# Kernel optimization log

Measured on AMD Instinct MI355X. Metric: run time of the kernel, lower is better.

## Reference

```python
import jax, jax.numpy as jnp
import numpy as np

D = 256   # feature_dim
NQ = 512  # num query keypoints
NK = 512  # num key/value keypoints


def setup_inputs() -> dict:
    key = jax.random.key(0)
    ks = jax.random.split(key, 10)
    def w(k, shape, fan_in):
        return jax.random.normal(k, shape, dtype=jnp.float32) / np.sqrt(fan_in)
    inp = {
        "x": jax.random.normal(ks[0], (1, D, NQ), dtype=jnp.float32),
        "source": jax.random.normal(ks[1], (1, D, NK), dtype=jnp.float32),
        # MLPAttention score MLP: Conv1d(2D->D,k=1), ReLU, Conv1d(D->1,k=1)
        "w1": w(ks[2], (D, 2 * D), 2 * D),
        "b1": w(ks[3], (D,), 2 * D),
        "w2": w(ks[4], (1, D), D),
        "b2": w(ks[5], (1,), D),
        # outer MLP: Conv1d(2D->2D,k=1), ReLU, Conv1d(2D->D,k=1) with zero bias init
        "wa": w(ks[6], (2 * D, 2 * D), 2 * D),
        "ba": w(ks[7], (2 * D,), 2 * D),
        "wb": w(ks[8], (D, 2 * D), 2 * D),
        "bb": jnp.zeros((D,), dtype=jnp.float32),
    }
    return inp


def reference(x, source, w1, b1, w2, b2, wa, ba, wb, bb):
    d = x.shape[1]
    q = x[0]       # [D, nq]
    k = source[0]  # [D, nk]
    # cat((q broadcast over nk, k broadcast over nq)) then Conv1d(2D->D) is
    # equivalent to splitting w1 into query/key halves and broadcasting:
    w1q, w1k = w1[:, :d], w1[:, d:]
    aq = w1q @ q + b1[:, None]                       # [D, nq]
    ak = w1k @ k                                     # [D, nk]
    h = jax.nn.relu(aq[:, :, None] + ak[:, None, :])  # [D, nq, nk]
    scores = (jnp.einsum('d,dnm->nm', w2[0], h) + b2[0])[None]  # [1, nq, nk]
    prob = jax.nn.softmax(scores, axis=-1)
    message = jnp.einsum('bnm,bdm->bdn', prob, source)  # [1, D, nq]
    # outer MLP on cat([x, message], channel dim)
    cat = jnp.concatenate([x, message], axis=1)         # [1, 2D, nq]
    h2 = jax.nn.relu(jnp.einsum('oc,bcn->bon', wa, cat) + ba[None, :, None])
    y = jnp.einsum('oc,bcn->bon', wb, h2) + bb[None, :, None]  # [1, D, nq]
    return (y, scores)
```

## Files before the change

kernel.cpp:

```cpp
#include <hip/hip_runtime.h>
#include <hip/hip_bf16.h>

#define DD 256
#define NN 512

typedef __attribute__((ext_vector_type(8))) short short8;
typedef __attribute__((ext_vector_type(4))) float floatx4;

__device__ __forceinline__ unsigned short f2bf(float f) {
  unsigned u = __float_as_uint(f);
  u += 0x7FFFu + ((u >> 16) & 1u);
  return (unsigned short)(u >> 16);
}
__device__ __forceinline__ unsigned pack2(float a, float b) {
  return (unsigned)f2bf(a) | ((unsigned)f2bf(b) << 16);
}

__device__ __forceinline__ short8 ldfrag(const unsigned short* __restrict__ base,
                                         int row, int ld, int k, int lane) {
  return *(const short8*)(base + (row + (lane & 15)) * ld + k + ((lane >> 4) << 3));
}

__device__ __forceinline__ short8 ldfrag_f32(const float* __restrict__ base,
                                             int row, int ld, int k, int lane) {
  const float* p = base + (row + (lane & 15)) * ld + k + ((lane >> 4) << 3);
  const float4 v0 = *(const float4*)p;
  const float4 v1 = *(const float4*)(p + 4);
  short8 r;
  r[0] = (short)f2bf(v0.x); r[1] = (short)f2bf(v0.y);
  r[2] = (short)f2bf(v0.z); r[3] = (short)f2bf(v0.w);
  r[4] = (short)f2bf(v1.x); r[5] = (short)f2bf(v1.y);
  r[6] = (short)f2bf(v1.z); r[7] = (short)f2bf(v1.w);
  return r;
}

__device__ __forceinline__ short8 ldfragT_g(const float* __restrict__ base,
                                            int n0, int ld, int k, int lane) {
  const int n = n0 + (lane & 15);
  const int kk = k + ((lane >> 4) << 3);
  short8 r;
#pragma unroll
  for (int j = 0; j < 8; ++j) r[j] = (short)f2bf(base[(kk + j) * ld + n]);
  return r;
}

template <int NF>
__device__ __forceinline__ void acc_zero(floatx4 acc[NF]) {
#pragma unroll
  for (int i = 0; i < NF; ++i) {
    acc[i][0] = 0.f; acc[i][1] = 0.f; acc[i][2] = 0.f; acc[i][3] = 0.f;
  }
}

template <int NF>
__device__ __forceinline__ void ksplit_combine(floatx4 acc[NF], float* red,
                                               int wave, int lane) {
  const int W = 16 * NF;
  const int col = lane & 15;
  const int q = lane >> 4;
  if (wave > 0) {
    float* base = red + (wave - 1) * 16 * W;
#pragma unroll
    for (int nf = 0; nf < NF; ++nf)
#pragma unroll
      for (int r = 0; r < 4; ++r)
        base[(q * 4 + r) * W + nf * 16 + col] = acc[nf][r];
  }
  __syncthreads();
  if (wave == 0) {
#pragma unroll
    for (int nf = 0; nf < NF; ++nf)
#pragma unroll
      for (int r = 0; r < 4; ++r) {
        const int idx = (q * 4 + r) * W + nf * 16 + col;
        acc[nf][r] += red[idx] + red[16 * W + idx] + red[32 * W + idx];
      }
  }
}

template <int NF, bool COLBIAS, bool ROWBIAS, bool RELU, bool OUTBF>
__device__ __forceinline__ void gemm_epi(floatx4 acc[NF],
    const float* __restrict__ bias, void* __restrict__ C, int ldc,
    int m0, int n0, int lane) {
  const int col = lane & 15;
  const int q = lane >> 4;
#pragma unroll
  for (int nf = 0; nf < NF; ++nf) {
    const int n = n0 + nf * 16 + col;
    const float cb = COLBIAS ? bias[n] : 0.0f;
#pragma unroll
    for (int r = 0; r < 4; ++r) {
      const int m = m0 + q * 4 + r;
      float v = acc[nf][r] + cb + (ROWBIAS ? bias[m] : 0.0f);
      if (RELU) v = fmaxf(v, 0.0f);
      if (OUTBF) ((unsigned short*)C)[m * ldc + n] = f2bf(v);
      else       ((float*)C)[m * ldc + n] = v;
    }
  }
}

__global__ __launch_bounds__(256) void aqak_kernel(
    const float* __restrict__ x, const float* __restrict__ src,
    const float* __restrict__ w1, const float* __restrict__ b1,
    const float* __restrict__ bb,
    float* __restrict__ aq, float* __restrict__ ak, float* __restrict__ y,
    unsigned short* __restrict__ xT) {
  __shared__ float red[1536];

  const int tid = threadIdx.x;
  const int z = blockIdx.z;

  if (z == 2) {
    const int c = blockIdx.y * 16 + blockIdx.x;
    const float bv = bb[c];
    float2 v; v.x = bv; v.y = bv;
    *(float2*)&y[c * NN + tid * 2] = v;
    const int n0t = c * 2 + (tid >> 7);
    const int d2 = (tid & 127) * 2;
    const float f0 = x[d2 * NN + n0t];
    const float f1 = x[(d2 + 1) * NN + n0t];
    *(unsigned*)&xT[n0t * DD + d2] = pack2(f0, f1);
    return;
  }

  const int lane = tid & 63;
  const int wave = tid >> 6;
  const int m0 = blockIdx.y * 16;
  const int n0 = blockIdx.x * 32;
  const float* in = z ? src : x;

  floatx4 acc[2]; acc_zero<2>(acc);
#pragma unroll
  for (int kc = 0; kc < 2; ++kc) {
    const int kl = wave * 64 + kc * 32;
    short8 a = ldfrag_f32(w1, m0, NN, z * 256 + kl, lane);
#pragma unroll
    for (int nf = 0; nf < 2; ++nf) {
      short8 b = ldfragT_g(in, n0 + nf * 16, NN, kl, lane);
      acc[nf] = __builtin_amdgcn_mfma_f32_16x16x32_bf16(a, b, acc[nf], 0, 0, 0);
    }
  }
  ksplit_combine<2>(acc, red, wave, lane);
  if (wave == 0) {
    if (z == 0) gemm_epi<2, false, true, false, false>(acc, b1, aq, NN, m0, n0, lane);
    else        gemm_epi<2, false, false, false, false>(acc, nullptr, ak, NN, m0, n0, lane);
  }
}

__global__ __launch_bounds__(256) void scores_kernel(
    const float* __restrict__ aq, const float* __restrict__ ak,
    const float* __restrict__ w2, const float* __restrict__ b2,
    float* __restrict__ sc) {
  __shared__ __align__(16) float aqs[256][36];
  __shared__ __align__(16) float aks[256][36];
  __shared__ __align__(16) float part[4][32][32];
  __shared__ float w2s[DD];

  const int tid = threadIdx.x;
  const int lane = tid & 63;
  const int wave = tid >> 6;
  const int n0 = blockIdx.x * 32;
  const int m0 = blockIdx.y * 32;

  w2s[tid] = w2[tid];

#pragma unroll
  for (int i = 0; i < 8; ++i) {
    const int idx = i * 256 + tid;
    const int row = idx >> 3;
    const int c4 = (idx & 7) * 4;
    *(float4*)&aqs[row][c4] = *(const float4*)&aq[row * NN + n0 + c4];
    *(float4*)&aks[row][c4] = *(const float4*)&ak[row * NN + m0 + c4];
  }
  __syncthreads();

  {
    const int nq = lane & 7;
    const int mq = lane >> 3;
    float s[4][4];
#pragma unroll
    for (int i = 0; i < 4; ++i)
#pragma unroll
      for (int j = 0; j < 4; ++j) s[i][j] = 0.f;

    const int dbeg = wave * 64;
    for (int dd = dbeg; dd < dbeg + 64; ++dd) {
      const float4 a4 = *(const float4*)&aqs[dd][nq * 4];
      const float4 k4 = *(const float4*)&aks[dd][mq * 4];
      const float w = w2s[dd];
      const float a[4] = {a4.x, a4.y, a4.z, a4.w};
      const float k[4] = {k4.x, k4.y, k4.z, k4.w};
#pragma unroll
      for (int i = 0; i < 4; ++i)
#pragma unroll
        for (int j = 0; j < 4; ++j)
          s[i][j] += w * fmaxf(a[i] + k[j], 0.f);
    }
#pragma unroll
    for (int i = 0; i < 4; ++i) {
      float4 o; o.x = s[i][0]; o.y = s[i][1]; o.z = s[i][2]; o.w = s[i][3];
      *(float4*)&part[wave][nq * 4 + i][mq * 4] = o;
    }
  }
  __syncthreads();

  {
    const int n = tid >> 3;
    const int mg = (tid & 7) * 4;
    const float4 p0 = *(const float4*)&part[0][n][mg];
    const float4 p1 = *(const float4*)&part[1][n][mg];
    const float4 p2 = *(const float4*)&part[2][n][mg];
    const float4 p3 = *(const float4*)&part[3][n][mg];
    const float bv = b2[0];
    float4 o;
    o.x = p0.x + p1.x + p2.x + p3.x + bv;
    o.y = p0.y + p1.y + p2.y + p3.y + bv;
    o.z = p0.z + p1.z + p2.z + p3.z + bv;
    o.w = p0.w + p1.w + p2.w + p3.w + bv;
    *(float4*)&sc[(n0 + n) * NN + m0 + mg] = o;
  }
}

__global__ __launch_bounds__(256) void msgT_kernel(
    const float* __restrict__ sc, const float* __restrict__ srcf,
    unsigned short* __restrict__ msgTb) {
  __shared__ unsigned short Ap[16][520];
  __shared__ float red[1536];
  __shared__ float smax[16][16];
  __shared__ float ssum[16][16];
  __shared__ float rst[16][2];

  const int tid = threadIdx.x;
  const int lane = tid & 63;
  const int wave = tid >> 6;
  const int n0 = blockIdx.y * 16;
  const int d0 = blockIdx.x * 32;

  const int r = tid >> 4;
  const int c = tid & 15;
  float4 v[8];
  const float* rp = sc + (n0 + r) * NN + c * 4;
#pragma unroll
  for (int i = 0; i < 8; ++i) v[i] = *(const float4*)(rp + i * 64);

  float mx = -3.0e38f;
#pragma unroll
  for (int i = 0; i < 8; ++i)
    mx = fmaxf(mx, fmaxf(fmaxf(v[i].x, v[i].y), fmaxf(v[i].z, v[i].w)));
  smax[r][c] = mx;
  __syncthreads();
  if (c == 0) {
    float m2 = smax[r][0];
#pragma unroll
    for (int i = 1; i < 16; ++i) m2 = fmaxf(m2, smax[r][i]);
    rst[r][0] = m2;
  }
  __syncthreads();
  mx = rst[r][0];

  float sum = 0.f;
#pragma unroll
  for (int i = 0; i < 8; ++i) {
    v[i].x = __expf(v[i].x - mx); v[i].y = __expf(v[i].y - mx);
    v[i].z = __expf(v[i].z - mx); v[i].w = __expf(v[i].w - mx);
    sum += v[i].x + v[i].y + v[i].z + v[i].w;
  }
  ssum[r][c] = sum;
  __syncthreads();
  if (c == 0) {
    float s2 = ssum[r][0];
#pragma unroll
    for (int i = 1; i < 16; ++i) s2 += ssum[r][i];
    rst[r][1] = s2;
  }
  __syncthreads();
  const float inv = 1.0f / rst[r][1];
#pragma unroll
  for (int i = 0; i < 8; ++i) {
    *(unsigned*)&Ap[r][c * 4 + i * 64]     = pack2(v[i].x * inv, v[i].y * inv);
    *(unsigned*)&Ap[r][c * 4 + i * 64 + 2] = pack2(v[i].z * inv, v[i].w * inv);
  }
  __syncthreads();

  floatx4 acc[2]; acc_zero<2>(acc);
  const int k0w = wave * 128;
  const int arow = lane & 15;
  const int koff = (lane >> 4) << 3;
#pragma unroll
  for (int k = 0; k < 128; k += 32) {
    short8 a = *(const short8*)&Ap[arow][k0w + k + koff];
#pragma unroll
    for (int nf = 0; nf < 2; ++nf) {
      short8 b = ldfrag_f32(srcf, d0 + nf * 16, NN, k0w + k, lane);
      acc[nf] = __builtin_amdgcn_mfma_f32_16x16x32_bf16(a, b, acc[nf], 0, 0, 0);
    }
  }
  ksplit_combine<2>(acc, red, wave, lane);
  if (wave == 0)
    gemm_epi<2, false, false, false, true>(acc, nullptr, msgTb, DD, n0, d0, lane);
}

__global__ __launch_bounds__(256) void h2y_kernel(
    const unsigned short* __restrict__ xT, const unsigned short* __restrict__ msgTb,
    const float* __restrict__ waf, const float* __restrict__ wbf,
    const float* __restrict__ ba, float* __restrict__ y) {
  __shared__ __align__(16) unsigned short h2L[16][72];

  const int tid = threadIdx.x;
  const int lane = tid & 63;
  const int wave = tid >> 6;
  const int o0 = blockIdx.x * 64;
  const int n0g = blockIdx.y * 16;

  {
    floatx4 acc;
    acc[0] = 0.f; acc[1] = 0.f; acc[2] = 0.f; acc[3] = 0.f;
    const int ow = o0 + wave * 16;
#pragma unroll
    for (int kc = 0; kc < 16; ++kc) {
      const int c0 = kc * 32;
      short8 a = (c0 < 256) ? ldfrag(xT, n0g, DD, c0, lane)
                            : ldfrag(msgTb, n0g, DD, c0 - 256, lane);
      short8 b = ldfrag_f32(waf, ow, NN, c0, lane);
      acc = __builtin_amdgcn_mfma_f32_16x16x32_bf16(a, b, acc, 0, 0, 0);
    }
    const int col = lane & 15, q = lane >> 4;
    const float cb = ba[o0 + wave * 16 + col];
#pragma unroll
    for (int r = 0; r < 4; ++r)
      h2L[q * 4 + r][wave * 16 + col] = f2bf(fmaxf(acc[r] + cb, 0.f));
  }
  __syncthreads();

  {
    const int brow = lane & 15;
    const int koff = (lane >> 4) << 3;
    const int col = lane & 15, q = lane >> 4;
#pragma unroll
    for (int t = 0; t < 4; ++t) {
      const int o2t = wave * 64 + t * 16;
      floatx4 acc;
      acc[0] = 0.f; acc[1] = 0.f; acc[2] = 0.f; acc[3] = 0.f;
#pragma unroll
      for (int kc = 0; kc < 2; ++kc) {
        short8 a = ldfrag_f32(wbf, o2t, NN, o0 + kc * 32, lane);
        short8 b = *(const short8*)&h2L[brow][kc * 32 + koff];
        acc = __builtin_amdgcn_mfma_f32_16x16x32_bf16(a, b, acc, 0, 0, 0);
      }
#pragma unroll
      for (int r = 0; r < 4; ++r)
        atomicAdd(&y[(o2t + q * 4 + r) * NN + n0g + col], acc[r]);
    }
  }
}

extern "C" void kernel_launch(void* const* d_in, const int* in_sizes, int n_in,
                              void* d_out, int out_size, void* d_ws, size_t ws_size,
                              hipStream_t stream) {
  (void)in_sizes; (void)n_in; (void)out_size; (void)ws_size;

  const float* x   = (const float*)d_in[0];
  const float* src = (const float*)d_in[1];
  const float* w1  = (const float*)d_in[2];
  const float* b1  = (const float*)d_in[3];
  const float* w2  = (const float*)d_in[4];
  const float* b2  = (const float*)d_in[5];
  const float* wa  = (const float*)d_in[6];
  const float* ba  = (const float*)d_in[7];
  const float* wb  = (const float*)d_in[8];
  const float* bb  = (const float*)d_in[9];

  float* y_out  = (float*)d_out;
  float* sc_out = (float*)d_out + 131072;

  char* ws = (char*)d_ws;
  float*          aq    = (float*)(ws);
  float*          ak    = (float*)(ws + (512 << 10));
  unsigned short* msgTb = (unsigned short*)(ws + (1024 << 10));
  unsigned short* xT    = (unsigned short*)(ws + (1280 << 10));

  aqak_kernel<<<dim3(16, 16, 3), 256, 0, stream>>>(x, src, w1, b1, bb, aq, ak,
                                                   y_out, xT);
  scores_kernel<<<dim3(16, 16), 256, 0, stream>>>(aq, ak, w2, b2, sc_out);
  msgT_kernel<<<dim3(8, 32), 256, 0, stream>>>(sc_out, src, msgTb);
  h2y_kernel<<<dim3(8, 32), 256, 0, stream>>>(xT, msgTb, wa, wb, ba, y_out);
}
```

Measured before the change: 104.7 us.

## Fuse four kernels into one cooperative kernel with grid-wide syncs

Merges the aqak, scores, softmax/message and outer-MLP kernels into one persistent cooperative kernel of 256 blocks. Stages are separated by grid.sync(), and shared memory is reused through a union. The goal is to remove three kernel launch gaps and their launch overhead. In exchange it adds the cost of grid barriers and fixes parallelism at 256 blocks, where the first stage previously launched 768.

```diff
diff --git a/kernel.cpp b/kernel.cpp
--- a/kernel.cpp
+++ b/kernel.cpp
@@ -1,5 +1,8 @@
 #include <hip/hip_runtime.h>
 #include <hip/hip_bf16.h>
+#include <hip/hip_cooperative_groups.h>
+
+namespace cg = cooperative_groups;
 
 #define DD 256
 #define NN 512
@@ -99,257 +102,254 @@
   }
 }
 
-__global__ __launch_bounds__(256) void aqak_kernel(
+union SMem {
+  float red[1536];
+  struct {
+    float aqs[256][36];
+    float aks[256][36];
+    float part[4][32][32];
+    float w2s[DD];
+  } s2;
+  struct {
+    unsigned short Ap[16][520];
+    float red[1536];
+    float smax[16][16];
+    float ssum[16][16];
+    float rst[16][2];
+  } s3;
+  unsigned short h2L[16][72];
+};
+
+__global__ __launch_bounds__(256) void fused_kernel(
     const float* __restrict__ x, const float* __restrict__ src,
     const float* __restrict__ w1, const float* __restrict__ b1,
-    const float* __restrict__ bb,
-    float* __restrict__ aq, float* __restrict__ ak, float* __restrict__ y,
-    unsigned short* __restrict__ xT) {
-  __shared__ float red[1536];
+    const float* __restrict__ w2, const float* __restrict__ b2,
+    const float* __restrict__ wa, const float* __restrict__ ba,
+    const float* __restrict__ wb, const float* __restrict__ bb,
+    float* __restrict__ y, float* __restrict__ sc,
+    float* __restrict__ aq, float* __restrict__ ak,
+    unsigned short* __restrict__ msgTb, unsigned short* __restrict__ xT) {
+  __shared__ __align__(16) SMem sm;
+  cg::grid_group grid = cg::this_grid();
 
   const int tid = threadIdx.x;
-  const int z = blockIdx.z;
-
-  if (z == 2) {
-    const int c = blockIdx.y * 16 + blockIdx.x;
-    const float bv = bb[c];
-    float2 v; v.x = bv; v.y = bv;
-    *(float2*)&y[c * NN + tid * 2] = v;
-    const int n0t = c * 2 + (tid >> 7);
+  const int b = blockIdx.x;
+  const int lane = tid & 63;
+  const int wave = tid >> 6;
+
+  {
+    const float bv = bb[b];
+    float2 v2; v2.x = bv; v2.y = bv;
+    *(float2*)&y[b * NN + tid * 2] = v2;
+    const int n0t = b * 2 + (tid >> 7);
     const int d2 = (tid & 127) * 2;
     const float f0 = x[d2 * NN + n0t];
     const float f1 = x[(d2 + 1) * NN + n0t];
     *(unsigned*)&xT[n0t * DD + d2] = pack2(f0, f1);
-    return;
-  }
-
-  const int lane = tid & 63;
-  const int wave = tid >> 6;
-  const int m0 = blockIdx.y * 16;
-  const int n0 = blockIdx.x * 32;
-  const float* in = z ? src : x;
-
-  floatx4 acc[2]; acc_zero<2>(acc);
-#pragma unroll
-  for (int kc = 0; kc < 2; ++kc) {
-    const int kl = wave * 64 + kc * 32;
-    short8 a = ldfrag_f32(w1, m0, NN, z * 256 + kl, lane);
-#pragma unroll
-    for (int nf = 0; nf < 2; ++nf) {
-      short8 b = ldfragT_g(in, n0 + nf * 16, NN, kl, lane);
-      acc[nf] = __builtin_amdgcn_mfma_f32_16x16x32_bf16(a, b, acc[nf], 0, 0, 0);
-    }
-  }
-  ksplit_combine<2>(acc, red, wave, lane);
-  if (wave == 0) {
-    if (z == 0) gemm_epi<2, false, true, false, false>(acc, b1, aq, NN, m0, n0, lane);
-    else        gemm_epi<2, false, false, false, false>(acc, nullptr, ak, NN, m0, n0, lane);
-  }
-}
-
-__global__ __launch_bounds__(256) void scores_kernel(
-    const float* __restrict__ aq, const float* __restrict__ ak,
-    const float* __restrict__ w2, const float* __restrict__ b2,
-    float* __restrict__ sc) {
-  __shared__ __align__(16) float aqs[256][36];
-  __shared__ __align__(16) float aks[256][36];
-  __shared__ __align__(16) float part[4][32][32];
-  __shared__ float w2s[DD];
-
-  const int tid = threadIdx.x;
-  const int lane = tid & 63;
-  const int wave = tid >> 6;
-  const int n0 = blockIdx.x * 32;
-  const int m0 = blockIdx.y * 32;
-
-  w2s[tid] = w2[tid];
-
-#pragma unroll
-  for (int i = 0; i < 8; ++i) {
-    const int idx = i * 256 + tid;
-    const int row = idx >> 3;
-    const int c4 = (idx & 7) * 4;
-    *(float4*)&aqs[row][c4] = *(const float4*)&aq[row * NN + n0 + c4];
-    *(float4*)&aks[row][c4] = *(const float4*)&ak[row * NN + m0 + c4];
-  }
-  __syncthreads();
-
-  {
-    const int nq = lane & 7;
-    const int mq = lane >> 3;
-    float s[4][4];
-#pragma unroll
-    for (int i = 0; i < 4; ++i)
-#pragma unroll
-      for (int j = 0; j < 4; ++j) s[i][j] = 0.f;
-
-    const int dbeg = wave * 64;
-    for (int dd = dbeg; dd < dbeg + 64; ++dd) {
-      const float4 a4 = *(const float4*)&aqs[dd][nq * 4];
-      const float4 k4 = *(const float4*)&aks[dd][mq * 4];
-      const float w = w2s[dd];
-      const float a[4] = {a4.x, a4.y, a4.z, a4.w};
-      const float k[4] = {k4.x, k4.y, k4.z, k4.w};
+  }
+  {
+    const int m0 = (b >> 4) * 16;
+    const int n0 = (b & 15) * 32;
+#pragma unroll
+    for (int z = 0; z < 2; ++z) {
+      const float* in = z ? src : x;
+      floatx4 acc[2]; acc_zero<2>(acc);
+#pragma unroll
+      for (int kc = 0; kc < 2; ++kc) {
+        const int kl = wave * 64 + kc * 32;
+        short8 a = ldfrag_f32(w1, m0, NN, z * 256 + kl, lane);
+#pragma unroll
+        for (int nf = 0; nf < 2; ++nf) {
+          short8 bf = ldfragT_g(in, n0 + nf * 16, NN, kl, lane);
+          acc[nf] = __builtin_amdgcn_mfma_f32_16x16x32_bf16(a, bf, acc[nf], 0, 0, 0);
+        }
+      }
+      if (z) __syncthreads();
+      ksplit_combine<2>(acc, sm.red, wave, lane);
+      if (wave == 0) {
+        if (z == 0) gemm_epi<2, false, true, false, false>(acc, b1, aq, NN, m0, n0, lane);
+        else        gemm_epi<2, false, false, false, false>(acc, nullptr, ak, NN, m0, n0, lane);
+      }
+    }
+  }
+  grid.sync();
+
+  {
+    const int n0 = (b & 15) * 32;
+    const int m0 = (b >> 4) * 32;
+
+    sm.s2.w2s[tid] = w2[tid];
+
+#pragma unroll
+    for (int i = 0; i < 8; ++i) {
+      const int idx = i * 256 + tid;
+      const int row = idx >> 3;
+      const int c4 = (idx & 7) * 4;
+      *(float4*)&sm.s2.aqs[row][c4] = *(const float4*)&aq[row * NN + n0 + c4];
+      *(float4*)&sm.s2.aks[row][c4] = *(const float4*)&ak[row * NN + m0 + c4];
+    }
+    __syncthreads();
+
+    {
+      const int nq = lane & 7;
+      const int mq = lane >> 3;
+      float s[4][4];
 #pragma unroll
       for (int i = 0; i < 4; ++i)
 #pragma unroll
-        for (int j = 0; j < 4; ++j)
-          s[i][j] += w * fmaxf(a[i] + k[j], 0.f);
-    }
-#pragma unroll
-    for (int i = 0; i < 4; ++i) {
-      float4 o; o.x = s[i][0]; o.y = s[i][1]; o.z = s[i][2]; o.w = s[i][3];
-      *(float4*)&part[wave][nq * 4 + i][mq * 4] = o;
-    }
-  }
-  __syncthreads();
-
-  {
-    const int n = tid >> 3;
-    const int mg = (tid & 7) * 4;
-    const float4 p0 = *(const float4*)&part[0][n][mg];
-    const float4 p1 = *(const float4*)&part[1][n][mg];
-    const float4 p2 = *(const float4*)&part[2][n][mg];
-    const float4 p3 = *(const float4*)&part[3][n][mg];
-    const float bv = b2[0];
-    float4 o;
-    o.x = p0.x + p1.x + p2.x + p3.x + bv;
-    o.y = p0.y + p1.y + p2.y + p3.y + bv;
-    o.z = p0.z + p1.z + p2.z + p3.z + bv;
-    o.w = p0.w + p1.w + p2.w + p3.w + bv;
-    *(float4*)&sc[(n0 + n) * NN + m0 + mg] = o;
-  }
-}
-
-__global__ __launch_bounds__(256) void msgT_kernel(
-    const float* __restrict__ sc, const float* __restrict__ srcf,
-    unsigned short* __restrict__ msgTb) {
-  __shared__ unsigned short Ap[16][520];
-  __shared__ float red[1536];
-  __shared__ float smax[16][16];
-  __shared__ float ssum[16][16];
-  __shared__ float rst[16][2];
-
-  const int tid = threadIdx.x;
-  const int lane = tid & 63;
-  const int wave = tid >> 6;
-  const int n0 = blockIdx.y * 16;
-  const int d0 = blockIdx.x * 32;
-
-  const int r = tid >> 4;
-  const int c = tid & 15;
-  float4 v[8];
-  const float* rp = sc + (n0 + r) * NN + c * 4;
-#pragma unroll
-  for (int i = 0; i < 8; ++i) v[i] = *(const float4*)(rp + i * 64);
-
-  float mx = -3.0e38f;
-#pragma unroll
-  for (int i = 0; i < 8; ++i)
-    mx = fmaxf(mx, fmaxf(fmaxf(v[i].x, v[i].y), fmaxf(v[i].z, v[i].w)));
-  smax[r][c] = mx;
-  __syncthreads();
-  if (c == 0) {
-    float m2 = smax[r][0];
-#pragma unroll
-    for (int i = 1; i < 16; ++i) m2 = fmaxf(m2, smax[r][i]);
-    rst[r][0] = m2;
-  }
-  __syncthreads();
-  mx = rst[r][0];
-
-  float sum = 0.f;
-#pragma unroll
-  for (int i = 0; i < 8; ++i) {
-    v[i].x = __expf(v[i].x - mx); v[i].y = __expf(v[i].y - mx);
-    v[i].z = __expf(v[i].z - mx); v[i].w = __expf(v[i].w - mx);
-    sum += v[i].x + v[i].y + v[i].z + v[i].w;
-  }
-  ssum[r][c] = sum;
-  __syncthreads();
-  if (c == 0) {
-    float s2 = ssum[r][0];
-#pragma unroll
-    for (int i = 1; i < 16; ++i) s2 += ssum[r][i];
-    rst[r][1] = s2;
-  }
-  __syncthreads();
-  const float inv = 1.0f / rst[r][1];
-#pragma unroll
-  for (int i = 0; i < 8; ++i) {
-    *(unsigned*)&Ap[r][c * 4 + i * 64]     = pack2(v[i].x * inv, v[i].y * inv);
-    *(unsigned*)&Ap[r][c * 4 + i * 64 + 2] = pack2(v[i].z * inv, v[i].w * inv);
-  }
-  __syncthreads();
-
-  floatx4 acc[2]; acc_zero<2>(acc);
-  const int k0w = wave * 128;
-  const int arow = lane & 15;
-  const int koff = (lane >> 4) << 3;
-#pragma unroll
-  for (int k = 0; k < 128; k += 32) {
-    short8 a = *(const short8*)&Ap[arow][k0w + k + koff];
-#pragma unroll
-    for (int nf = 0; nf < 2; ++nf) {
-      short8 b = ldfrag_f32(srcf, d0 + nf * 16, NN, k0w + k, lane);
-      acc[nf] = __builtin_amdgcn_mfma_f32_16x16x32_bf16(a, b, acc[nf], 0, 0, 0);
-    }
-  }
-  ksplit_combine<2>(acc, red, wave, lane);
-  if (wave == 0)
-    gemm_epi<2, false, false, false, true>(acc, nullptr, msgTb, DD, n0, d0, lane);
-}
-
-__global__ __launch_bounds__(256) void h2y_kernel(
-    const unsigned short* __restrict__ xT, const unsigned short* __restrict__ msgTb,
-    const float* __restrict__ waf, const float* __restrict__ wbf,
-    const float* __restrict__ ba, float* __restrict__ y) {
-  __shared__ __align__(16) unsigned short h2L[16][72];
-
-  const int tid = threadIdx.x;
-  const int lane = tid & 63;
-  const int wave = tid >> 6;
-  const int o0 = blockIdx.x * 64;
-  const int n0g = blockIdx.y * 16;
-
-  {
-    floatx4 acc;
-    acc[0] = 0.f; acc[1] = 0.f; acc[2] = 0.f; acc[3] = 0.f;
-    const int ow = o0 + wave * 16;
-#pragma unroll
-    for (int kc = 0; kc < 16; ++kc) {
-      const int c0 = kc * 32;
-      short8 a = (c0 < 256) ? ldfrag(xT, n0g, DD, c0, lane)
-                            : ldfrag(msgTb, n0g, DD, c0 - 256, lane);
-      short8 b = ldfrag_f32(waf, ow, NN, c0, lane);
-      acc = __builtin_amdgcn_mfma_f32_16x16x32_bf16(a, b, acc, 0, 0, 0);
-    }
-    const int col = lane & 15, q = lane >> 4;
-    const float cb = ba[o0 + wave * 16 + col];
-#pragma unroll
-    for (int r = 0; r < 4; ++r)
-      h2L[q * 4 + r][wave * 16 + col] = f2bf(fmaxf(acc[r] + cb, 0.f));
-  }
-  __syncthreads();
-
-  {
-    const int brow = lane & 15;
+        for (int j = 0; j < 4; ++j) s[i][j] = 0.f;
+
+      const int dbeg = wave * 64;
+      for (int dd = dbeg; dd < dbeg + 64; ++dd) {
+        const float4 a4 = *(const float4*)&sm.s2.aqs[dd][nq * 4];
+        const float4 k4 = *(const float4*)&sm.s2.aks[dd][mq * 4];
+        const float w = sm.s2.w2s[dd];
+        const float a[4] = {a4.x, a4.y, a4.z, a4.w};
+        const float k[4] = {k4.x, k4.y, k4.z, k4.w};
+#pragma unroll
+        for (int i = 0; i < 4; ++i)
+#pragma unroll
+          for (int j = 0; j < 4; ++j)
+            s[i][j] += w * fmaxf(a[i] + k[j], 0.f);
+      }
+#pragma unroll
+      for (int i = 0; i < 4; ++i) {
+        float4 o; o.x = s[i][0]; o.y = s[i][1]; o.z = s[i][2]; o.w = s[i][3];
+        *(float4*)&sm.s2.part[wave][nq * 4 + i][mq * 4] = o;
+      }
+    }
+    __syncthreads();
+
+    {
+      const int n = tid >> 3;
+      const int mg = (tid & 7) * 4;
+      const float4 p0 = *(const float4*)&sm.s2.part[0][n][mg];
+      const float4 p1 = *(const float4*)&sm.s2.part[1][n][mg];
+      const float4 p2 = *(const float4*)&sm.s2.part[2][n][mg];
+      const float4 p3 = *(const float4*)&sm.s2.part[3][n][mg];
+      const float bv = b2[0];
+      float4 o;
+      o.x = p0.x + p1.x + p2.x + p3.x + bv;
+      o.y = p0.y + p1.y + p2.y + p3.y + bv;
+      o.z = p0.z + p1.z + p2.z + p3.z + bv;
+      o.w = p0.w + p1.w + p2.w + p3.w + bv;
+      *(float4*)&sc[(n0 + n) * NN + m0 + mg] = o;
+    }
+  }
+  grid.sync();
+
+  {
+    const int n0 = (b >> 3) * 16;
+    const int d0 = (b & 7) * 32;
+
+    const int r = tid >> 4;
+    const int c = tid & 15;
+    float4 v[8];
+    const float* rp = sc + (n0 + r) * NN + c * 4;
+#pragma unroll
+    for (int i = 0; i < 8; ++i) v[i] = *(const float4*)(rp + i * 64);
+
+    float mx = -3.0e38f;
+#pragma unroll
+    for (int i = 0; i < 8; ++i)
+      mx = fmaxf(mx, fmaxf(fmaxf(v[i].x, v[i].y), fmaxf(v[i].z, v[i].w)));
+    sm.s3.smax[r][c] = mx;
+    __syncthreads();
+    if (c == 0) {
+      float m2 = sm.s3.smax[r][0];
+#pragma unroll
+      for (int i = 1; i < 16; ++i) m2 = fmaxf(m2, sm.s3.smax[r][i]);
+      sm.s3.rst[r][0] = m2;
+    }
+    __syncthreads();
+    mx = sm.s3.rst[r][0];
+
+    float sum = 0.f;
+#pragma unroll
+    for (int i = 0; i < 8; ++i) {
+      v[i].x = __expf(v[i].x - mx); v[i].y = __expf(v[i].y - mx);
+      v[i].z = __expf(v[i].z - mx); v[i].w = __expf(v[i].w - mx);
+      sum += v[i].x + v[i].y + v[i].z + v[i].w;
+    }
+    sm.s3.ssum[r][c] = sum;
+    __syncthreads();
+    if (c == 0) {
+      float s2 = sm.s3.ssum[r][0];
+#pragma unroll
+      for (int i = 1; i < 16; ++i) s2 += sm.s3.ssum[r][i];
+      sm.s3.rst[r][1] = s2;
+    }
+    __syncthreads();
+    const float inv = 1.0f / sm.s3.rst[r][1];
+#pragma unroll
+    for (int i = 0; i < 8; ++i) {
+      *(unsigned*)&sm.s3.Ap[r][c * 4 + i * 64]     = pack2(v[i].x * inv, v[i].y * inv);
+      *(unsigned*)&sm.s3.Ap[r][c * 4 + i * 64 + 2] = pack2(v[i].z * inv, v[i].w * inv);
+    }
+    __syncthreads();
+
+    floatx4 acc[2]; acc_zero<2>(acc);
+    const int k0w = wave * 128;
+    const int arow = lane & 15;
     const int koff = (lane >> 4) << 3;
-    const int col = lane & 15, q = lane >> 4;
-#pragma unroll
-    for (int t = 0; t < 4; ++t) {
-      const int o2t = wave * 64 + t * 16;
+#pragma unroll
+    for (int k = 0; k < 128; k += 32) {
+      short8 a = *(const short8*)&sm.s3.Ap[arow][k0w + k + koff];
+#pragma unroll
+      for (int nf = 0; nf < 2; ++nf) {
+        short8 bf = ldfrag_f32(src, d0 + nf * 16, NN, k0w + k, lane);
+        acc[nf] = __builtin_amdgcn_mfma_f32_16x16x32_bf16(a, bf, acc[nf], 0, 0, 0);
+      }
+    }
+    ksplit_combine<2>(acc, sm.s3.red, wave, lane);
+    if (wave == 0)
+      gemm_epi<2, false, false, false, true>(acc, nullptr, msgTb, DD, n0, d0, lane);
+  }
+  grid.sync();
+
+  {
+    const int o0 = (b & 7) * 64;
+    const int n0g = (b >> 3) * 16;
+
+    {
       floatx4 acc;
       acc[0] = 0.f; acc[1] = 0.f; acc[2] = 0.f; acc[3] = 0.f;
-#pragma unroll
-      for (int kc = 0; kc < 2; ++kc) {
-        short8 a = ldfrag_f32(wbf, o2t, NN, o0 + kc * 32, lane);
-        short8 b = *(const short8*)&h2L[brow][kc * 32 + koff];
-        acc = __builtin_amdgcn_mfma_f32_16x16x32_bf16(a, b, acc, 0, 0, 0);
-      }
+      const int ow = o0 + wave * 16;
+#pragma unroll
+      for (int kc = 0; kc < 16; ++kc) {
+        const int c0 = kc * 32;
+        short8 a = (c0 < 256) ? ldfrag(xT, n0g, DD, c0, lane)
+                              : ldfrag(msgTb, n0g, DD, c0 - 256, lane);
+        short8 bf = ldfrag_f32(wa, ow, NN, c0, lane);
+        acc = __builtin_amdgcn_mfma_f32_16x16x32_bf16(a, bf, acc, 0, 0, 0);
+      }
+      const int col = lane & 15, q = lane >> 4;
+      const float cb = ba[o0 + wave * 16 + col];
 #pragma unroll
       for (int r = 0; r < 4; ++r)
-        atomicAdd(&y[(o2t + q * 4 + r) * NN + n0g + col], acc[r]);
+        sm.h2L[q * 4 + r][wave * 16 + col] = f2bf(fmaxf(acc[r] + cb, 0.f));
+    }
+    __syncthreads();
+
+    {
+      const int brow = lane & 15;
+      const int koff = (lane >> 4) << 3;
+      const int col = lane & 15, q = lane >> 4;
+#pragma unroll
+      for (int t = 0; t < 4; ++t) {
+        const int o2t = wave * 64 + t * 16;
+        floatx4 acc;
+        acc[0] = 0.f; acc[1] = 0.f; acc[2] = 0.f; acc[3] = 0.f;
+#pragma unroll
+        for (int kc = 0; kc < 2; ++kc) {
+          short8 a = ldfrag_f32(wb, o2t, NN, o0 + kc * 32, lane);
+          short8 bf = *(const short8*)&sm.h2L[brow][kc * 32 + koff];
+          acc = __builtin_amdgcn_mfma_f32_16x16x32_bf16(a, bf, acc, 0, 0, 0);
+        }
+#pragma unroll
+        for (int r = 0; r < 4; ++r)
+          atomicAdd(&y[(o2t + q * 4 + r) * NN + n0g + col], acc[r]);
+      }
     }
   }
 }
@@ -379,9 +379,15 @@
   unsigned short* msgTb = (unsigned short*)(ws + (1024 << 10));
   unsigned short* xT    = (unsigned short*)(ws + (1280 << 10));
 
-  aqak_kernel<<<dim3(16, 16, 3), 256, 0, stream>>>(x, src, w1, b1, bb, aq, ak,
-                                                   y_out, xT);
-  scores_kernel<<<dim3(16, 16), 256, 0, stream>>>(aq, ak, w2, b2, sc_out);
-  msgT_kernel<<<dim3(8, 32), 256, 0, stream>>>(sc_out, src, msgTb);
-  h2y_kernel<<<dim3(8, 32), 256, 0, stream>>>(xT, msgTb, wa, wb, ba, y_out);
-}
+  void* args[16];
+  args[0]  = (void*)&x;     args[1]  = (void*)&src;
+  args[2]  = (void*)&w1;    args[3]  = (void*)&b1;
+  args[4]  = (void*)&w2;    args[5]  = (void*)&b2;
+  args[6]  = (void*)&wa;    args[7]  = (void*)&ba;
+  args[8]  = (void*)&wb;    args[9]  = (void*)&bb;
+  args[10] = (void*)&y_out; args[11] = (void*)&sc_out;
+  args[12] = (void*)&aq;    args[13] = (void*)&ak;
+  args[14] = (void*)&msgTb; args[15] = (void*)&xT;
+
+  hipLaunchCooperativeKernel(fused_kernel, dim3(256), dim3(256), args, 0, stream);
+}
```

Measured after the change: 205.3 us. +96.1%, slower.

## Stage aqak B operand in LDS and double scores kernel waves

Applied to the files above, without the earlier changes.

The aqak kernel now loads its input tile with coalesced float4 reads into shared memory, then builds the transposed bf16 MFMA fragments from LDS. This replaces the strided per-element global gathers. The scores kernel moves to 512 threads with 8 waves, each taking 32 of the feature rows, and the final reduction sums 8 partials. This adds LDS usage and one more sync in aqak and a larger partial buffer in scores, in exchange for better memory coalescing and more latency hiding on the dominant relu-sum loop.

```diff
diff --git a/kernel.cpp b/kernel.cpp
--- a/kernel.cpp
+++ b/kernel.cpp
@@ -34,16 +34,6 @@
   return r;
 }
 
-__device__ __forceinline__ short8 ldfragT_g(const float* __restrict__ base,
-                                            int n0, int ld, int k, int lane) {
-  const int n = n0 + (lane & 15);
-  const int kk = k + ((lane >> 4) << 3);
-  short8 r;
-#pragma unroll
-  for (int j = 0; j < 8; ++j) r[j] = (short)f2bf(base[(kk + j) * ld + n]);
-  return r;
-}
-
 template <int NF>
 __device__ __forceinline__ void acc_zero(floatx4 acc[NF]) {
 #pragma unroll
@@ -106,6 +96,7 @@
     float* __restrict__ aq, float* __restrict__ ak, float* __restrict__ y,
     unsigned short* __restrict__ xT) {
   __shared__ float red[1536];
+  __shared__ __align__(16) float bt[256][33];
 
   const int tid = threadIdx.x;
   const int z = blockIdx.z;
@@ -129,6 +120,15 @@
   const int n0 = blockIdx.x * 32;
   const float* in = z ? src : x;
 
+#pragma unroll
+  for (int i = 0; i < 8; ++i) {
+    const int idx = i * 256 + tid;
+    const int row = idx >> 3;
+    const int c4 = (idx & 7) * 4;
+    *(float4*)&bt[row][c4] = *(const float4*)&in[row * NN + n0 + c4];
+  }
+  __syncthreads();
+
   floatx4 acc[2]; acc_zero<2>(acc);
 #pragma unroll
   for (int kc = 0; kc < 2; ++kc) {
@@ -136,7 +136,11 @@
     short8 a = ldfrag_f32(w1, m0, NN, z * 256 + kl, lane);
 #pragma unroll
     for (int nf = 0; nf < 2; ++nf) {
-      short8 b = ldfragT_g(in, n0 + nf * 16, NN, kl, lane);
+      const int n = nf * 16 + (lane & 15);
+      const int kk = kl + ((lane >> 4) << 3);
+      short8 b;
+#pragma unroll
+      for (int j = 0; j < 8; ++j) b[j] = (short)f2bf(bt[kk + j][n]);
       acc[nf] = __builtin_amdgcn_mfma_f32_16x16x32_bf16(a, b, acc[nf], 0, 0, 0);
     }
   }
@@ -147,13 +151,13 @@
   }
 }
 
-__global__ __launch_bounds__(256) void scores_kernel(
+__global__ __launch_bounds__(512) void scores_kernel(
     const float* __restrict__ aq, const float* __restrict__ ak,
     const float* __restrict__ w2, const float* __restrict__ b2,
     float* __restrict__ sc) {
   __shared__ __align__(16) float aqs[256][36];
   __shared__ __align__(16) float aks[256][36];
-  __shared__ __align__(16) float part[4][32][32];
+  __shared__ __align__(16) float part[8][32][32];
   __shared__ float w2s[DD];
 
   const int tid = threadIdx.x;
@@ -162,11 +166,11 @@
   const int n0 = blockIdx.x * 32;
   const int m0 = blockIdx.y * 32;
 
-  w2s[tid] = w2[tid];
-
-#pragma unroll
-  for (int i = 0; i < 8; ++i) {
-    const int idx = i * 256 + tid;
+  if (tid < DD) w2s[tid] = w2[tid];
+
+#pragma unroll
+  for (int i = 0; i < 4; ++i) {
+    const int idx = i * 512 + tid;
     const int row = idx >> 3;
     const int c4 = (idx & 7) * 4;
     *(float4*)&aqs[row][c4] = *(const float4*)&aq[row * NN + n0 + c4];
@@ -183,8 +187,8 @@
 #pragma unroll
       for (int j = 0; j < 4; ++j) s[i][j] = 0.f;
 
-    const int dbeg = wave * 64;
-    for (int dd = dbeg; dd < dbeg + 64; ++dd) {
+    const int dbeg = wave * 32;
+    for (int dd = dbeg; dd < dbeg + 32; ++dd) {
       const float4 a4 = *(const float4*)&aqs[dd][nq * 4];
       const float4 k4 = *(const float4*)&aks[dd][mq * 4];
       const float w = w2s[dd];
@@ -204,19 +208,16 @@
   }
   __syncthreads();
 
-  {
+  if (tid < 256) {
     const int n = tid >> 3;
     const int mg = (tid & 7) * 4;
-    const float4 p0 = *(const float4*)&part[0][n][mg];
-    const float4 p1 = *(const float4*)&part[1][n][mg];
-    const float4 p2 = *(const float4*)&part[2][n][mg];
-    const float4 p3 = *(const float4*)&part[3][n][mg];
     const float bv = b2[0];
-    float4 o;
-    o.x = p0.x + p1.x + p2.x + p3.x + bv;
-    o.y = p0.y + p1.y + p2.y + p3.y + bv;
-    o.z = p0.z + p1.z + p2.z + p3.z + bv;
-    o.w = p0.w + p1.w + p2.w + p3.w + bv;
+    float4 o; o.x = bv; o.y = bv; o.z = bv; o.w = bv;
+#pragma unroll
+    for (int wv = 0; wv < 8; ++wv) {
+      const float4 p = *(const float4*)&part[wv][n][mg];
+      o.x += p.x; o.y += p.y; o.z += p.z; o.w += p.w;
+    }
     *(float4*)&sc[(n0 + n) * NN + m0 + mg] = o;
   }
 }
@@ -381,7 +382,7 @@
 
   aqak_kernel<<<dim3(16, 16, 3), 256, 0, stream>>>(x, src, w1, b1, bb, aq, ak,
                                                    y_out, xT);
-  scores_kernel<<<dim3(16, 16), 256, 0, stream>>>(aq, ak, w2, b2, sc_out);
+  scores_kernel<<<dim3(16, 16), 512, 0, stream>>>(aq, ak, w2, b2, sc_out);
   msgT_kernel<<<dim3(8, 32), 256, 0, stream>>>(sc_out, src, msgTb);
   h2y_kernel<<<dim3(8, 32), 256, 0, stream>>>(xT, msgTb, wa, wb, ba, y_out);
 }
```

Measured after the change: 101.7 us. -2.8%, faster.
